# Performance work log

Measured on AMD Instinct MI355X. Metric: run time of the kernel, lower is better.

## Reference

```python
import jax, jax.numpy as jnp
import numpy as np

K = 3
PAD = 1


def conv3x3(x, w, b):
    # x: [B,Ci,H,W], w: [Co,Ci,3,3] -> [B,Co,H,W]
    y = jax.lax.conv_general_dilated(
        x, w, window_strides=(1, 1), padding=((PAD, PAD), (PAD, PAD)),
        dimension_numbers=('NCHW', 'OIHW', 'NCHW'))
    return y + b[None, :, None, None]


def _gather(x_flat, idx):
    # x_flat: [C, H*W], idx: [K2*H*W] -> [C, K2*H*W]
    return x_flat[:, idx]


def deform_sample(x, off_x, off_y, mask):
    """Modulated deformable im2col (DCNv2, dg=1, stride=1, pad=1, dil=1).
    x: [B,C,H,W]; off_x, off_y, mask: [B,K2,H,W] -> cols [B,C,K2,H,W]."""
    B, C, H, W = x.shape
    K2 = K * K
    # static kernel-tap displacements relative to output pixel
    dy = jnp.repeat(jnp.arange(K), K) - PAD          # [K2]
    dx = jnp.tile(jnp.arange(K), K) - PAD            # [K2]
    gy = jnp.arange(H)[:, None].astype(x.dtype)      # [H,1]
    gx = jnp.arange(W)[None, :].astype(x.dtype)      # [1,W]
    ys = gy[None, None] + dy[None, :, None, None].astype(x.dtype) + off_y  # [B,K2,H,W]
    xs = gx[None, None] + dx[None, :, None, None].astype(x.dtype) + off_x
    y0 = jnp.floor(ys)
    x0 = jnp.floor(xs)
    wy1 = ys - y0
    wx1 = xs - x0
    xf = x.reshape(B, C, H * W)
    val = jnp.zeros((B, C, K2, H, W), x.dtype)
    for oy, ox in ((0, 0), (0, 1), (1, 0), (1, 1)):
        yy = y0 + oy
        xx = x0 + ox
        wgt = (wy1 if oy else 1.0 - wy1) * (wx1 if ox else 1.0 - wx1)
        valid = ((yy >= 0) & (yy < H) & (xx >= 0) & (xx < W)).astype(x.dtype)
        idx = (jnp.clip(yy, 0, H - 1) * W + jnp.clip(xx, 0, W - 1)).astype(jnp.int32)
        g = jax.vmap(_gather)(xf, idx.reshape(B, -1)).reshape(B, C, K2, H, W)
        val = val + (wgt * valid)[:, None] * g
    return val * mask[:, None]  # modulation, broadcast over C


def reference(x, feat, w_off, b_off, w_def, b_def):
    # offset/mask prediction conv (3*K2 channels), chunked as in the torch module
    om = conv3x3(feat, w_off, b_off)
    off_x, off_y, m = jnp.split(om, 3, axis=1)   # each [B,K2,H,W]
    mask = jax.nn.sigmoid(m)
    cols = deform_sample(x, off_x, off_y, mask)  # [B,C,K2,H,W]
    O = w_def.shape[0]
    out = jnp.einsum('bckhw,ock->bohw', cols, w_def.reshape(O, -1, K * K))
    out = out + b_def[None, :, None, None]
    return jax.nn.relu(out)


def setup_inputs() -> dict:
    key = jax.random.key(0)
    k1, k2, k3, k4 = jax.random.split(key, 4)
    B, C, O, H, W = 4, 64, 64, 128, 128
    K2 = K * K
    x = jax.random.normal(k1, (B, C, H, W), jnp.float32)
    feat = jax.random.normal(k2, (B, C, H, W), jnp.float32)
    # offset conv params: small init so offsets stay near zero (as in practice)
    w_off = jax.random.normal(k3, (3 * K2, C, 3, 3), jnp.float32) * 0.01
    b_off = jnp.zeros((3 * K2,), jnp.float32)
    w_def = jax.random.normal(k4, (O, C, 3, 3), jnp.float32) * (1.0 / np.sqrt(C * K2))
    b_def = jnp.zeros((O,), jnp.float32)
    return {"x": x, "feat": feat, "w_off": w_off, "b_off": b_off,
            "w_def": w_def, "b_def": b_def}
```

## Files before the change

kernel.cpp:

```cpp
#include <hip/hip_runtime.h>
#include <math.h>

#define Bn 4
#define Cn 64
#define On 64
#define Hn 128
#define Wn 128
#define HWn (Hn * Wn)

typedef __attribute__((ext_vector_type(8))) short s16x8;
typedef __attribute__((ext_vector_type(4))) float f32x4;

__device__ __forceinline__ unsigned short f2bf(float f) {
    unsigned u = __float_as_uint(f);
    u += 0x7fffu + ((u >> 16) & 1u);
    return (unsigned short)(u >> 16);
}
__device__ __forceinline__ float bf2f(unsigned short u) {
    return __uint_as_float(((unsigned)u) << 16);
}

__global__ __launch_bounds__(256) void transpose_all(const float* __restrict__ x,
                                                     const float* __restrict__ feat,
                                                     const float* __restrict__ wdef,
                                                     const float* __restrict__ woff,
                                                     ushort* __restrict__ xt,
                                                     ushort* __restrict__ ft,
                                                     ushort* __restrict__ wdT2,
                                                     ushort* __restrict__ woT2) {
    int t = threadIdx.x;
    if (blockIdx.z == 2) {
        int id = (blockIdx.y * gridDim.x + blockIdx.x) * 256 + t;
        if (id < 36864) {
            int c2 = id & 31, oc = (id >> 5) & 63, ks = id >> 11;
            int k = ks % 9, s = ks / 9;
            wdT2[id] = f2bf(wdef[(oc * 64 + s * 32 + c2) * 9 + k]);
        } else if (id < 55296) {
            int i2 = id - 36864;
            int c2 = i2 & 31, oc = (i2 >> 5) & 31, ks = i2 >> 10;
            int k = ks % 9, s = ks / 9;
            woT2[i2] = (oc < 27) ? f2bf(woff[(oc * 64 + s * 32 + c2) * 9 + k]) : (ushort)0;
        }
        return;
    }
    __shared__ float tile[64][65];
    const float* src = blockIdx.z ? feat : x;
    ushort* dst0 = blockIdx.z ? ft : xt;
    int b = blockIdx.y, hw0 = blockIdx.x * 64;
    int lane = t & 63, grp = t >> 6;
    const float* xb = src + (size_t)b * Cn * HWn;
#pragma unroll
    for (int i = 0; i < 16; ++i) {
        int c = grp * 16 + i;
        tile[lane][c] = xb[(size_t)c * HWn + hw0 + lane];
    }
    __syncthreads();
#pragma unroll
    for (int jj = 0; jj < 2; ++jj) {
        int px = jj * 32 + (t >> 3), ch = t & 7;
        s16x8 p;
#pragma unroll
        for (int j = 0; j < 8; ++j) p[j] = (short)f2bf(tile[px][ch * 8 + j]);
        *(s16x8*)(dst0 + ((size_t)(b * HWn + hw0 + px)) * Cn + ch * 8) = p;
    }
}

__global__ __launch_bounds__(256, 4) void off_conv_kernel(const ushort* __restrict__ ft,
                                                          const ushort* __restrict__ woT2,
                                                          const float* __restrict__ b_off,
                                                          float* __restrict__ om) {
    __shared__ __align__(16) char smem[26624];
    ushort* s_win = (ushort*)smem;
    float* s_out = (float*)smem;

    int t = threadIdx.x;
    int wv = t >> 6, l = t & 63;
    int q = l >> 4, r = l & 15;
    int h = blockIdx.x >> 1, wb = (blockIdx.x & 1) * 64;
    int b = blockIdx.y;
    const ushort* ft_b = ft + (size_t)b * HWn * Cn;

#pragma unroll
    for (int i = 0; i < 7; ++i) {
        int jb = i * 256 + wv * 64;
        if (jb < 1664) {
            int j = jb + l;
            int lin = j >> 3, slot = j & 7;
            int linc = min(lin, 203);
            int cidx = (slot - lin) & 7;
            int row = linc / 68, col = linc - row * 68;
            int rs = min(max(h - 1 + row, 0), Hn - 1);
            int cs = min(max(wb - 1 + col, 0), Wn - 1);
            const ushort* gp = ft_b + (size_t)(rs * Wn + cs) * Cn + cidx * 8;
            __builtin_amdgcn_global_load_lds(
                (const __attribute__((address_space(1))) unsigned int*)gp,
                (__attribute__((address_space(3))) unsigned int*)(s_win + (size_t)jb * 8),
                16, 0, 0);
        }
    }
    __syncthreads();

    f32x4 zero = {0.f, 0.f, 0.f, 0.f};
    s16x8 zz = {0, 0, 0, 0, 0, 0, 0, 0};
    f32x4 acc[2];
    acc[0] = zero; acc[1] = zero;

    int px = wv * 16 + r;
#pragma unroll 3
    for (int k = 0; k < 9; ++k) {
        int dy = k / 3 - 1, dx = k % 3 - 1;
        int y = h + dy;
        bool yv = (y >= 0) && (y < Hn);
        int xx = wb + px + dx;
        bool valid = yv && (xx >= 0) && (xx < Wn);
        int lin = (dy + 1) * 68 + px + dx + 1;
#pragma unroll
        for (int s = 0; s < 2; ++s) {
            int c = s * 4 + q;
            s16x8 av = *(const s16x8*)&s_win[lin * 64 + (((c + lin) & 7) << 3)];
            av = valid ? av : zz;
#pragma unroll
            for (int ot = 0; ot < 2; ++ot) {
                s16x8 bv = *(const s16x8*)(woT2 + (size_t)s * 9216
                                           + (size_t)(k * 32 + ot * 16 + r) * 32 + q * 8);
                acc[ot] = __builtin_amdgcn_mfma_f32_16x16x32_bf16(av, bv, acc[ot], 0, 0, 0);
            }
        }
    }
    __syncthreads();

#pragma unroll
    for (int ot = 0; ot < 2; ++ot) {
        int oc = ot * 16 + r;
        float bo = (oc < 27) ? b_off[oc] : 0.f;
#pragma unroll
        for (int reg = 0; reg < 4; ++reg) {
            int p = wv * 16 + q * 4 + reg;
            float v = acc[ot][reg] + bo;
            if (oc >= 18 && oc < 27) v = 1.f / (1.f + __expf(-v));
            s_out[oc * 68 + p] = v;
        }
    }
    __syncthreads();
    for (int idx = t; idx < 27 * 64; idx += 256) {
        int o = idx >> 6, p = idx & 63;
        om[((size_t)b * 27 + o) * HWn + h * Wn + wb + p] = s_out[o * 68 + p];
    }
}

__global__ __launch_bounds__(256, 3) void mega_kernel(const ushort* __restrict__ xt,
                                                      const ushort* __restrict__ wdT2,
                                                      const float* __restrict__ om,
                                                      const float* __restrict__ b_def,
                                                      float* __restrict__ out) {
    __shared__ __align__(16) char smem[28672];
    ushort* s_win = (ushort*)smem;
    float* s_out = (float*)smem;

    int t = threadIdx.x;
    int wv = t >> 6, l = t & 63;
    int q = l >> 4, r = l & 15;
    int blk = (blockIdx.x & 7) * 128 + (blockIdx.x >> 3);
    int b = blk >> 8;
    int gi = blk & 255;
    int h = (gi >> 2) << 1;
    int wbase = (gi & 3) << 5;
    int rowoff = wv >> 1, pxh = wv & 1;
    int hrow = h + rowoff;
    int pxi = pxh * 16 + r;
    float pxif = (float)pxi;
    float rowofff = (float)rowoff;
    const ushort* xt_b = xt + (size_t)b * HWn * Cn;

#pragma unroll
    for (int i = 0; i < 7; ++i) {
        int jb = i * 256 + wv * 64;
        int j = jb + l;
        int lin = j >> 3, slot = j & 7;
        int linc = min(lin, 215);
        int cidx = (slot - lin) & 7;
        int row = linc / 36, col = linc - row * 36;
        int rs = min(max(h - 2 + row, 0), Hn - 1);
        int cs = min(max(wbase - 2 + col, 0), Wn - 1);
        const ushort* gp = xt_b + (size_t)(rs * Wn + cs) * Cn + cidx * 8;
        __builtin_amdgcn_global_load_lds(
            (const __attribute__((address_space(1))) unsigned int*)gp,
            (__attribute__((address_space(3))) unsigned int*)(s_win + (size_t)jb * 8),
            16, 0, 0);
    }

    const float* om_b = om + ((size_t)b * 27) * HWn + hrow * Wn + wbase + pxi;
    float omv[27];
#pragma unroll
    for (int o = 0; o < 27; ++o) omv[o] = om_b[(size_t)o * HWn];

    bool okp = true;
#pragma unroll
    for (int k = 0; k < 9; ++k) {
        float uy = (float)(k / 3 - 1) + omv[9 + k];
        float ux = pxif + (float)(k % 3 - 1) + omv[k];
        okp = okp && (uy >= -2.f - rowofff) && (uy < 3.f - rowofff)
                  && (ux >= -2.f) && (ux < 33.f);
    }
    int fast = __all(okp) ? 1 : 0;

    __syncthreads();

    f32x4 zero = {0.f, 0.f, 0.f, 0.f};
    f32x4 acc[4];
    acc[0] = zero; acc[1] = zero; acc[2] = zero; acc[3] = zero;

    if (fast) {
#pragma unroll 3
        for (int k = 0; k < 9; ++k) {
            float uy = (float)(k / 3 - 1) + omv[9 + k];
            float ux = pxif + (float)(k % 3 - 1) + omv[k];
            float mv = omv[18 + k];
            float y0f = floorf(uy), x0f = floorf(ux);
            float fy = uy - y0f, fx = ux - x0f;
            int iy = (int)y0f + 2 + rowoff;
            int ix = (int)x0f + 2;
            int yab = hrow + (int)y0f, xab = wbase + (int)x0f;
            bool vy0 = (yab >= 0) && (yab < Hn);
            bool vy1 = (yab + 1 >= 0) && (yab + 1 < Hn);
            bool vx0 = (xab >= 0) && (xab < Wn);
            bool vx1 = (xab + 1 >= 0) && (xab + 1 < Wn);
            float g0 = (vy0 && vx0) ? (1.f - fy) * (1.f - fx) * mv : 0.f;
            float g1 = (vy0 && vx1) ? (1.f - fy) * fx * mv : 0.f;
            float g2 = (vy1 && vx0) ? fy * (1.f - fx) * mv : 0.f;
            float g3 = (vy1 && vx1) ? fy * fx * mv : 0.f;
            int l0 = iy * 36 + ix, l1 = l0 + 1, l2 = l0 + 36, l3 = l0 + 37;
            s16x8 bw[2][4];
#pragma unroll
            for (int s = 0; s < 2; ++s)
#pragma unroll
                for (int ot = 0; ot < 4; ++ot)
                    bw[s][ot] = *(const s16x8*)(wdT2 + (size_t)s * 18432
                                                + (size_t)(k * 64 + ot * 16 + r) * 32 + q * 8);
            s16x8 af[2];
#pragma unroll
            for (int s = 0; s < 2; ++s) {
                int c = s * 4 + q;
                s16x8 q0 = *(const s16x8*)&s_win[l0 * 64 + (((c + l0) & 7) << 3)];
                s16x8 q1 = *(const s16x8*)&s_win[l1 * 64 + (((c + l1) & 7) << 3)];
                s16x8 q2 = *(const s16x8*)&s_win[l2 * 64 + (((c + l2) & 7) << 3)];
                s16x8 q3 = *(const s16x8*)&s_win[l3 * 64 + (((c + l3) & 7) << 3)];
                s16x8 p;
#pragma unroll
                for (int j = 0; j < 8; ++j) {
                    float rr = g0 * bf2f((unsigned short)q0[j]) + g1 * bf2f((unsigned short)q1[j])
                             + g2 * bf2f((unsigned short)q2[j]) + g3 * bf2f((unsigned short)q3[j]);
                    p[j] = (short)f2bf(rr);
                }
                af[s] = p;
            }
#pragma unroll
            for (int s = 0; s < 2; ++s)
#pragma unroll
                for (int ot = 0; ot < 4; ++ot)
                    acc[ot] = __builtin_amdgcn_mfma_f32_16x16x32_bf16(af[s], bw[s][ot], acc[ot], 0, 0, 0);
        }
    } else {
#pragma unroll 1
        for (int k = 0; k < 9; ++k) {
            float ys = (float)(hrow + k / 3 - 1) + omv[9 + k];
            float xs = (float)(wbase + pxi + k % 3 - 1) + omv[k];
            float mv = omv[18 + k];
            float y0f = floorf(ys), x0f = floorf(xs);
            float fy = ys - y0f, fx = xs - x0f;
            int y0 = (int)y0f, x0 = (int)x0f;
            float g[4];
            int a[4];
#pragma unroll
            for (int n = 0; n < 4; ++n) {
                int yy = y0 + (n >> 1), xx = x0 + (n & 1);
                bool valid = (yy >= 0) && (yy < Hn) && (xx >= 0) && (xx < Wn);
                float wgt = ((n >> 1) ? fy : 1.f - fy) * ((n & 1) ? fx : 1.f - fx) * mv;
                g[n] = valid ? wgt : 0.f;
                int yc = min(max(yy, 0), Hn - 1), xc = min(max(xx, 0), Wn - 1);
                a[n] = (yc * Wn + xc) * Cn;
            }
#pragma unroll
            for (int s = 0; s < 2; ++s) {
                int c = s * 32 + q * 8;
                s16x8 q0 = *(const s16x8*)(xt_b + a[0] + c);
                s16x8 q1 = *(const s16x8*)(xt_b + a[1] + c);
                s16x8 q2 = *(const s16x8*)(xt_b + a[2] + c);
                s16x8 q3 = *(const s16x8*)(xt_b + a[3] + c);
                s16x8 af;
#pragma unroll
                for (int j = 0; j < 8; ++j) {
                    float rr = g[0] * bf2f((unsigned short)q0[j]) + g[1] * bf2f((unsigned short)q1[j])
                             + g[2] * bf2f((unsigned short)q2[j]) + g[3] * bf2f((unsigned short)q3[j]);
                    af[j] = (short)f2bf(rr);
                }
#pragma unroll
                for (int ot = 0; ot < 4; ++ot) {
                    s16x8 bv = *(const s16x8*)(wdT2 + (size_t)s * 18432
                                               + (size_t)(k * 64 + ot * 16 + r) * 32 + q * 8);
                    acc[ot] = __builtin_amdgcn_mfma_f32_16x16x32_bf16(af, bv, acc[ot], 0, 0, 0);
                }
            }
        }
    }
    __syncthreads();

#pragma unroll
    for (int ot = 0; ot < 4; ++ot) {
        int oc = ot * 16 + r;
        float bv = b_def[oc];
        f32x4 vv;
#pragma unroll
        for (int reg = 0; reg < 4; ++reg) vv[reg] = fmaxf(acc[ot][reg] + bv, 0.f);
        *(f32x4*)&s_out[oc * 68 + rowoff * 32 + pxh * 16 + q * 4] = vv;
    }
    __syncthreads();
    {
        int px = t & 63, og = t >> 6;
        int rg = h + (px >> 5);
        float* ob = out + ((size_t)b * On) * HWn + rg * Wn + wbase + (px & 31);
#pragma unroll
        for (int j = 0; j < 16; ++j) {
            int oc = og * 16 + j;
            ob[(size_t)oc * HWn] = s_out[oc * 68 + px];
        }
    }
}

extern "C" void kernel_launch(void* const* d_in, const int* in_sizes, int n_in,
                              void* d_out, int out_size, void* d_ws, size_t ws_size,
                              hipStream_t stream) {
    const float* x = (const float*)d_in[0];
    const float* feat = (const float*)d_in[1];
    const float* w_off = (const float*)d_in[2];
    const float* b_off = (const float*)d_in[3];
    const float* w_def = (const float*)d_in[4];
    const float* b_def = (const float*)d_in[5];
    float* out = (float*)d_out;

    char* ws = (char*)d_ws;
    ushort* xt = (ushort*)ws;
    ushort* ft = (ushort*)(ws + 8388608);
    ushort* wdT2 = (ushort*)(ws + 16777216);
    ushort* woT2 = (ushort*)(ws + 16850944);
    float* om = (float*)(ws + 16887808);

    hipLaunchKernelGGL(transpose_all, dim3(HWn / 64, Bn, 3), dim3(256), 0, stream,
                       x, feat, w_def, w_off, xt, ft, wdT2, woT2);
    hipLaunchKernelGGL(off_conv_kernel, dim3(Hn * 2, Bn), dim3(256), 0, stream,
                       ft, woT2, b_off, om);
    hipLaunchKernelGGL(mega_kernel, dim3((Bn * HWn) / 64), dim3(256), 0, stream,
                       xt, wdT2, om, b_def, out);
}
```

Baseline: 131.5 us.

## Fuse offset/mask conv into deformable mega kernel, dropping om round-trip

Removes the separate offset-prediction conv kernel and computes the 27-channel offset/mask conv inside the main deformable kernel for each 2x32 tile, staging a feat halo window in shared memory and keeping results in LDS instead of writing and re-reading a global om buffer. This saves one launch and the global traffic for om. In exchange, shared memory per block grows from 28 KB to 46 KB, which may lower occupancy. Each block also re-reads overlapping feat halo rows, and a partial vmcnt wait is used to overlap the x-window loads with the offset conv.

```diff
diff --git a/kernel.cpp b/kernel.cpp
--- a/kernel.cpp
+++ b/kernel.cpp
@@ -65,97 +65,18 @@
     }
 }
 
-__global__ __launch_bounds__(256, 4) void off_conv_kernel(const ushort* __restrict__ ft,
-                                                          const ushort* __restrict__ woT2,
-                                                          const float* __restrict__ b_off,
-                                                          float* __restrict__ om) {
-    __shared__ __align__(16) char smem[26624];
-    ushort* s_win = (ushort*)smem;
-    float* s_out = (float*)smem;
-
-    int t = threadIdx.x;
-    int wv = t >> 6, l = t & 63;
-    int q = l >> 4, r = l & 15;
-    int h = blockIdx.x >> 1, wb = (blockIdx.x & 1) * 64;
-    int b = blockIdx.y;
-    const ushort* ft_b = ft + (size_t)b * HWn * Cn;
-
-#pragma unroll
-    for (int i = 0; i < 7; ++i) {
-        int jb = i * 256 + wv * 64;
-        if (jb < 1664) {
-            int j = jb + l;
-            int lin = j >> 3, slot = j & 7;
-            int linc = min(lin, 203);
-            int cidx = (slot - lin) & 7;
-            int row = linc / 68, col = linc - row * 68;
-            int rs = min(max(h - 1 + row, 0), Hn - 1);
-            int cs = min(max(wb - 1 + col, 0), Wn - 1);
-            const ushort* gp = ft_b + (size_t)(rs * Wn + cs) * Cn + cidx * 8;
-            __builtin_amdgcn_global_load_lds(
-                (const __attribute__((address_space(1))) unsigned int*)gp,
-                (__attribute__((address_space(3))) unsigned int*)(s_win + (size_t)jb * 8),
-                16, 0, 0);
-        }
-    }
-    __syncthreads();
-
-    f32x4 zero = {0.f, 0.f, 0.f, 0.f};
-    s16x8 zz = {0, 0, 0, 0, 0, 0, 0, 0};
-    f32x4 acc[2];
-    acc[0] = zero; acc[1] = zero;
-
-    int px = wv * 16 + r;
-#pragma unroll 3
-    for (int k = 0; k < 9; ++k) {
-        int dy = k / 3 - 1, dx = k % 3 - 1;
-        int y = h + dy;
-        bool yv = (y >= 0) && (y < Hn);
-        int xx = wb + px + dx;
-        bool valid = yv && (xx >= 0) && (xx < Wn);
-        int lin = (dy + 1) * 68 + px + dx + 1;
-#pragma unroll
-        for (int s = 0; s < 2; ++s) {
-            int c = s * 4 + q;
-            s16x8 av = *(const s16x8*)&s_win[lin * 64 + (((c + lin) & 7) << 3)];
-            av = valid ? av : zz;
-#pragma unroll
-            for (int ot = 0; ot < 2; ++ot) {
-                s16x8 bv = *(const s16x8*)(woT2 + (size_t)s * 9216
-                                           + (size_t)(k * 32 + ot * 16 + r) * 32 + q * 8);
-                acc[ot] = __builtin_amdgcn_mfma_f32_16x16x32_bf16(av, bv, acc[ot], 0, 0, 0);
-            }
-        }
-    }
-    __syncthreads();
-
-#pragma unroll
-    for (int ot = 0; ot < 2; ++ot) {
-        int oc = ot * 16 + r;
-        float bo = (oc < 27) ? b_off[oc] : 0.f;
-#pragma unroll
-        for (int reg = 0; reg < 4; ++reg) {
-            int p = wv * 16 + q * 4 + reg;
-            float v = acc[ot][reg] + bo;
-            if (oc >= 18 && oc < 27) v = 1.f / (1.f + __expf(-v));
-            s_out[oc * 68 + p] = v;
-        }
-    }
-    __syncthreads();
-    for (int idx = t; idx < 27 * 64; idx += 256) {
-        int o = idx >> 6, p = idx & 63;
-        om[((size_t)b * 27 + o) * HWn + h * Wn + wb + p] = s_out[o * 68 + p];
-    }
-}
-
 __global__ __launch_bounds__(256, 3) void mega_kernel(const ushort* __restrict__ xt,
+                                                      const ushort* __restrict__ ft,
                                                       const ushort* __restrict__ wdT2,
-                                                      const float* __restrict__ om,
+                                                      const ushort* __restrict__ woT2,
+                                                      const float* __restrict__ b_off,
                                                       const float* __restrict__ b_def,
                                                       float* __restrict__ out) {
-    __shared__ __align__(16) char smem[28672];
+    __shared__ __align__(16) char smem[47104];
     ushort* s_win = (ushort*)smem;
-    float* s_out = (float*)smem;
+    ushort* s_ft = (ushort*)(smem + 28672);
+    float* s_om = (float*)(smem + 28672);
+    float* s_out = (float*)(smem + 28672);
 
     int t = threadIdx.x;
     int wv = t >> 6, l = t & 63;
@@ -171,7 +92,25 @@
     float pxif = (float)pxi;
     float rowofff = (float)rowoff;
     const ushort* xt_b = xt + (size_t)b * HWn * Cn;
-
+    const ushort* ft_b = ft + (size_t)b * HWn * Cn;
+
+#pragma unroll
+    for (int i = 0; i < 5; ++i) {
+        int jb = i * 256 + wv * 64;
+        if (jb < 1152) {
+            int j = jb + l;
+            int lin = j >> 3, slot = j & 7;
+            int cidx = (slot - lin) & 7;
+            int row = lin / 36, col = lin - row * 36;
+            int rs = min(max(h - 1 + row, 0), Hn - 1);
+            int cs = min(max(wbase - 2 + col, 0), Wn - 1);
+            const ushort* gp = ft_b + (size_t)(rs * Wn + cs) * Cn + cidx * 8;
+            __builtin_amdgcn_global_load_lds(
+                (const __attribute__((address_space(1))) unsigned int*)gp,
+                (__attribute__((address_space(3))) unsigned int*)(s_ft + (size_t)jb * 8),
+                16, 0, 0);
+        }
+    }
 #pragma unroll
     for (int i = 0; i < 7; ++i) {
         int jb = i * 256 + wv * 64;
@@ -188,12 +127,60 @@
             (__attribute__((address_space(3))) unsigned int*)(s_win + (size_t)jb * 8),
             16, 0, 0);
     }
-
-    const float* om_b = om + ((size_t)b * 27) * HWn + hrow * Wn + wbase + pxi;
+    asm volatile("s_waitcnt vmcnt(7)" ::: "memory");
+    __builtin_amdgcn_s_barrier();
+
+    f32x4 zero = {0.f, 0.f, 0.f, 0.f};
+    s16x8 zz = {0, 0, 0, 0, 0, 0, 0, 0};
+
+    f32x4 acc2[2];
+    acc2[0] = zero; acc2[1] = zero;
+    {
+        int pxg = wv * 16 + r;
+        int rg = pxg >> 5, cg = pxg & 31;
+#pragma unroll 3
+        for (int k = 0; k < 9; ++k) {
+            int dy = k / 3 - 1, dx = k % 3 - 1;
+            int y = h + rg + dy;
+            bool yv = (y >= 0) && (y < Hn);
+            int xx = wbase + cg + dx;
+            bool valid = yv && (xx >= 0) && (xx < Wn);
+            int lin = (rg + dy + 1) * 36 + cg + dx + 2;
+#pragma unroll
+            for (int s = 0; s < 2; ++s) {
+                int c = s * 4 + q;
+                s16x8 av = *(const s16x8*)&s_ft[lin * 64 + (((c + lin) & 7) << 3)];
+                av = valid ? av : zz;
+#pragma unroll
+                for (int ot = 0; ot < 2; ++ot) {
+                    s16x8 bv = *(const s16x8*)(woT2 + (size_t)s * 9216
+                                               + (size_t)(k * 32 + ot * 16 + r) * 32 + q * 8);
+                    acc2[ot] = __builtin_amdgcn_mfma_f32_16x16x32_bf16(av, bv, acc2[ot], 0, 0, 0);
+                }
+            }
+        }
+    }
+    __syncthreads();
+
+#pragma unroll
+    for (int ot = 0; ot < 2; ++ot) {
+        int oc = ot * 16 + r;
+        if (oc < 27) {
+            float bo = b_off[oc];
+#pragma unroll
+            for (int reg = 0; reg < 4; ++reg) {
+                int p = wv * 16 + q * 4 + reg;
+                float v = acc2[ot][reg] + bo;
+                if (oc >= 18) v = 1.f / (1.f + __expf(-v));
+                s_om[oc * 64 + p] = v;
+            }
+        }
+    }
+    __syncthreads();
+
     float omv[27];
 #pragma unroll
-    for (int o = 0; o < 27; ++o) omv[o] = om_b[(size_t)o * HWn];
-
+    for (int o = 0; o < 27; ++o) omv[o] = s_om[o * 64 + rowoff * 32 + pxi];
     bool okp = true;
 #pragma unroll
     for (int k = 0; k < 9; ++k) {
@@ -204,9 +191,6 @@
     }
     int fast = __all(okp) ? 1 : 0;
 
-    __syncthreads();
-
-    f32x4 zero = {0.f, 0.f, 0.f, 0.f};
     f32x4 acc[4];
     acc[0] = zero; acc[1] = zero; acc[2] = zero; acc[3] = zero;
 
@@ -343,12 +327,9 @@
     ushort* ft = (ushort*)(ws + 8388608);
     ushort* wdT2 = (ushort*)(ws + 16777216);
     ushort* woT2 = (ushort*)(ws + 16850944);
-    float* om = (float*)(ws + 16887808);
 
     hipLaunchKernelGGL(transpose_all, dim3(HWn / 64, Bn, 3), dim3(256), 0, stream,
                        x, feat, w_def, w_off, xt, ft, wdT2, woT2);
-    hipLaunchKernelGGL(off_conv_kernel, dim3(Hn * 2, Bn), dim3(256), 0, stream,
-                       ft, woT2, b_off, om);
     hipLaunchKernelGGL(mega_kernel, dim3((Bn * HWn) / 64), dim3(256), 0, stream,
-                       xt, wdT2, om, b_def, out);
-}
+                       xt, ft, wdT2, woT2, b_off, b_def, out);
+}
```

New measurement: 123.0 us. 6.5% less time.
